# Kernel tuning notes

Measured on AMD Instinct MI355X. Metric: run time of the kernel, lower is better.

## Reference

```python
import jax, jax.numpy as jnp
import numpy as np

LR = 0.1  # inner-loop learning rate from `param - 0.1 * grad`

D = 4096          # memory width d; key/val are (1, d) per docstring
CTX = 512         # loss_context_size: number of keys per update step


def setup_inputs() -> dict:
    key = jax.random.key(0)
    k1, k2, k3 = jax.random.split(key, 3)
    W = jax.random.normal(k1, (D, D), dtype=jnp.float32) / np.sqrt(D)
    keys = jax.random.normal(k2, (CTX, D), dtype=jnp.float32)
    vals = jax.random.normal(k3, (CTX, D), dtype=jnp.float32)
    return {"W": W, "keys": keys, "vals": vals}


def reference(W, keys, vals):
    # OneStep.forward: preds_i = functional_forward(key_i, (W,)) = key_i @ W,
    # loss = MSE(preds, vals); new_W = W - 0.1 * dloss/dW.
    # The per-key loop is batched into a single (CTX, D) x (D, D) matmul.
    def loss_fn(Wp):
        preds = keys @ Wp  # (CTX, D)
        return jnp.mean((preds - vals) ** 2)

    g = jax.grad(loss_fn)(W)
    return W - LR * g
```

## Files before the change

kernel.cpp:

```cpp
#include <hip/hip_runtime.h>
#include <hip/hip_bf16.h>


typedef __bf16 bf16_t;
typedef __bf16 bf16x8 __attribute__((ext_vector_type(8)));
typedef float f32x4 __attribute__((ext_vector_type(4)));

#define D_DIM 4096
#define CTX_N 512
#define UPD_SCALE 9.5367431640625e-8f

__device__ __forceinline__ void gld16(const bf16_t* g, bf16_t* l) {
    __builtin_amdgcn_global_load_lds(
        (const __attribute__((address_space(1))) void*)g,
        (__attribute__((address_space(3))) void*)l, 16, 0, 0);
}

__global__ __launch_bounds__(256) void t_conv(
    const float* __restrict__ src, bf16_t* __restrict__ dstT,
    bf16_t* __restrict__ dstN, int M, int N)
{
    __shared__ float tile[64 * 65];
    const int tid = threadIdx.x;
    const int C0 = blockIdx.x * 64;
    const int R0 = blockIdx.y * 64;
    const int r  = tid >> 2, cs = (tid & 3) * 16;

    const float* s = src + (size_t)(R0 + r) * N + C0 + cs;
    float f[16];
#pragma unroll
    for (int u = 0; u < 4; ++u) {
        const float4 v = ((const float4*)s)[u];
        f[4 * u + 0] = v.x; f[4 * u + 1] = v.y; f[4 * u + 2] = v.z; f[4 * u + 3] = v.w;
    }
#pragma unroll
    for (int u = 0; u < 16; ++u) tile[r * 65 + cs + u] = f[u];

    if (dstN) {
        bf16x8 v0, v1;
#pragma unroll
        for (int u = 0; u < 8; ++u) { v0[u] = (bf16_t)f[u]; v1[u] = (bf16_t)f[8 + u]; }
        bf16_t* d = dstN + (size_t)(R0 + r) * N + C0 + cs;
        *(bf16x8*)d = v0; *(bf16x8*)(d + 8) = v1;
    }
    __syncthreads();

    const int rr = tid >> 2, k0 = (tid & 3) * 16;
    bf16x8 o0, o1;
#pragma unroll
    for (int u = 0; u < 8; ++u) {
        o0[u] = (bf16_t)tile[(k0 + u) * 65 + rr];
        o1[u] = (bf16_t)tile[(k0 + 8 + u) * 65 + rr];
    }
    bf16_t* d = dstT + (size_t)(C0 + rr) * M + R0 + k0;
    *(bf16x8*)d = o0; *(bf16x8*)(d + 8) = o1;
}

__global__ __launch_bounds__(256) void k1_residual(
    const bf16_t* __restrict__ Wt, const bf16_t* __restrict__ Kb,
    const bf16_t* __restrict__ Vt, bf16_t* __restrict__ Rt)
{
    __shared__ __align__(16) bf16_t As[64 * 32];
    __shared__ __align__(16) bf16_t Bs[64 * 32];

    const int tid = threadIdx.x;
    const int j0 = blockIdx.x * 64;
    const int c0 = blockIdx.y * 64;
    const int lane = tid & 63, wave = tid >> 6;
    const int wm = (wave >> 1) * 32, wn = (wave & 1) * 32;
    const int l15 = lane & 15, quad = lane >> 4;

    f32x4 acc[2][2] = {};

    const int srow = tid >> 2, sseg = (tid & 3) * 8;
    const bf16_t* ga = Wt + (size_t)(j0 + srow) * D_DIM + sseg;
    const bf16_t* gb = Kb + (size_t)(c0 + srow) * D_DIM + sseg;
    bf16_t* la = (bf16_t*)((char*)As + tid * 16);
    bf16_t* lb = (bf16_t*)((char*)Bs + tid * 16);

    for (int kk = 0; kk < D_DIM; kk += 32) {
        gld16(ga + kk, la);
        gld16(gb + kk, lb);
        __syncthreads();
        const bf16x8 a0 = *(const bf16x8*)(As + (wm + 0  + l15) * 32 + quad * 8);
        const bf16x8 a1 = *(const bf16x8*)(As + (wm + 16 + l15) * 32 + quad * 8);
        const bf16x8 b0 = *(const bf16x8*)(Bs + (wn + 0  + l15) * 32 + quad * 8);
        const bf16x8 b1 = *(const bf16x8*)(Bs + (wn + 16 + l15) * 32 + quad * 8);
        acc[0][0] = __builtin_amdgcn_mfma_f32_16x16x32_bf16(a0, b0, acc[0][0], 0, 0, 0);
        acc[0][1] = __builtin_amdgcn_mfma_f32_16x16x32_bf16(a0, b1, acc[0][1], 0, 0, 0);
        acc[1][0] = __builtin_amdgcn_mfma_f32_16x16x32_bf16(a1, b0, acc[1][0], 0, 0, 0);
        acc[1][1] = __builtin_amdgcn_mfma_f32_16x16x32_bf16(a1, b1, acc[1][1], 0, 0, 0);
        __syncthreads();
    }

#pragma unroll
    for (int im = 0; im < 2; ++im)
#pragma unroll
        for (int in = 0; in < 2; ++in)
#pragma unroll
            for (int r = 0; r < 4; ++r) {
                const int j = j0 + wm + im * 16 + quad * 4 + r;
                const int c = c0 + wn + in * 16 + l15;
                const size_t idx = (size_t)j * CTX_N + c;
                Rt[idx] = (bf16_t)(acc[im][in][r] - (float)Vt[idx]);
            }
}

__global__ __launch_bounds__(256) void k2_update(
    const bf16_t* __restrict__ Kt, const bf16_t* __restrict__ Rt,
    const float* __restrict__ W, float* __restrict__ out)
{
    __shared__ __align__(16) bf16_t As[64 * 32];
    __shared__ __align__(16) bf16_t Bs[64 * 32];

    const int tid = threadIdx.x;
    const int j0 = blockIdx.x * 64;
    const int i0 = blockIdx.y * 64;
    const int lane = tid & 63, wave = tid >> 6;
    const int wm = (wave >> 1) * 32, wn = (wave & 1) * 32;
    const int l15 = lane & 15, quad = lane >> 4;

    f32x4 acc[2][2] = {};

    const int srow = tid >> 2, sseg = (tid & 3) * 8;
    const bf16_t* ga = Kt + (size_t)(i0 + srow) * CTX_N + sseg;
    const bf16_t* gb = Rt + (size_t)(j0 + srow) * CTX_N + sseg;
    bf16_t* la = (bf16_t*)((char*)As + tid * 16);
    bf16_t* lb = (bf16_t*)((char*)Bs + tid * 16);

    for (int cc = 0; cc < CTX_N; cc += 32) {
        gld16(ga + cc, la);
        gld16(gb + cc, lb);
        __syncthreads();
        const bf16x8 a0 = *(const bf16x8*)(As + (wm + 0  + l15) * 32 + quad * 8);
        const bf16x8 a1 = *(const bf16x8*)(As + (wm + 16 + l15) * 32 + quad * 8);
        const bf16x8 b0 = *(const bf16x8*)(Bs + (wn + 0  + l15) * 32 + quad * 8);
        const bf16x8 b1 = *(const bf16x8*)(Bs + (wn + 16 + l15) * 32 + quad * 8);
        acc[0][0] = __builtin_amdgcn_mfma_f32_16x16x32_bf16(a0, b0, acc[0][0], 0, 0, 0);
        acc[0][1] = __builtin_amdgcn_mfma_f32_16x16x32_bf16(a0, b1, acc[0][1], 0, 0, 0);
        acc[1][0] = __builtin_amdgcn_mfma_f32_16x16x32_bf16(a1, b0, acc[1][0], 0, 0, 0);
        acc[1][1] = __builtin_amdgcn_mfma_f32_16x16x32_bf16(a1, b1, acc[1][1], 0, 0, 0);
        __syncthreads();
    }

#pragma unroll
    for (int im = 0; im < 2; ++im)
#pragma unroll
        for (int in = 0; in < 2; ++in)
#pragma unroll
            for (int r = 0; r < 4; ++r) {
                const int i = i0 + wm + im * 16 + quad * 4 + r;
                const int j = j0 + wn + in * 16 + l15;
                const size_t idx = (size_t)i * D_DIM + j;
                out[idx] = W[idx] - UPD_SCALE * acc[im][in][r];
            }
}

extern "C" void kernel_launch(void* const* d_in, const int* in_sizes, int n_in,
                              void* d_out, int out_size, void* d_ws, size_t ws_size,
                              hipStream_t stream) {
    const float* W = (const float*)d_in[0];
    const float* K = (const float*)d_in[1];
    const float* V = (const float*)d_in[2];
    float* out = (float*)d_out;

    char* ws = (char*)d_ws;
    bf16_t* Wt = (bf16_t*)(ws);
    bf16_t* Kt = (bf16_t*)(ws + (size_t)32 * 1024 * 1024);
    bf16_t* Kb = (bf16_t*)(ws + (size_t)36 * 1024 * 1024);
    bf16_t* Vt = (bf16_t*)(ws + (size_t)40 * 1024 * 1024);
    bf16_t* Rt = (bf16_t*)(ws + (size_t)44 * 1024 * 1024);

    t_conv<<<dim3(64, 64), 256, 0, stream>>>(W, Wt, nullptr, D_DIM, D_DIM);
    t_conv<<<dim3(64, 8),  256, 0, stream>>>(K, Kt, Kb,      CTX_N, D_DIM);
    t_conv<<<dim3(64, 8),  256, 0, stream>>>(V, Vt, nullptr, CTX_N, D_DIM);
    k1_residual<<<dim3(64, 8),  256, 0, stream>>>(Wt, Kb, Vt, Rt);
    k2_update  <<<dim3(64, 64), 256, 0, stream>>>(Kt, Rt, W, out);
}
```

Baseline: 231.3 us.

## Enlarge GEMM tiles, stage update epilogue via LDS, merge K/V conversion launches

The residual GEMM now uses 128x64 tiles with a 64-wide k step, and the update GEMM uses 128x128 tiles with 4x4 MFMA fragments per wave. This gives more data reuse per LDS load and fewer block launches. The update epilogue stages accumulators through shared memory so W reads and output writes are coalesced float4 accesses. The K and V transpose-convert launches are merged into one grid. In exchange, register and LDS use rise, which lowers occupancy, and the residual GEMM now has only 256 blocks.

```diff
diff --git a/kernel.cpp b/kernel.cpp
--- a/kernel.cpp
+++ b/kernel.cpp
@@ -16,7 +16,7 @@
         (__attribute__((address_space(3))) void*)l, 16, 0, 0);
 }
 
-__global__ __launch_bounds__(256) void t_conv(
+__device__ __forceinline__ void t_body(
     const float* __restrict__ src, bf16_t* __restrict__ dstT,
     bf16_t* __restrict__ dstN, int M, int N)
 {
@@ -45,64 +45,89 @@
     }
     __syncthreads();
 
-    const int rr = tid >> 2, k0 = (tid & 3) * 16;
     bf16x8 o0, o1;
 #pragma unroll
     for (int u = 0; u < 8; ++u) {
-        o0[u] = (bf16_t)tile[(k0 + u) * 65 + rr];
-        o1[u] = (bf16_t)tile[(k0 + 8 + u) * 65 + rr];
-    }
-    bf16_t* d = dstT + (size_t)(C0 + rr) * M + R0 + k0;
+        o0[u] = (bf16_t)tile[(cs + u) * 65 + r];
+        o1[u] = (bf16_t)tile[(cs + 8 + u) * 65 + r];
+    }
+    bf16_t* d = dstT + (size_t)(C0 + r) * M + R0 + cs;
     *(bf16x8*)d = o0; *(bf16x8*)(d + 8) = o1;
 }
+
+__global__ __launch_bounds__(256) void t_conv_w(
+    const float* __restrict__ W, bf16_t* __restrict__ Wt)
+{
+    t_body(W, Wt, nullptr, D_DIM, D_DIM);
+}
+
+__global__ __launch_bounds__(256) void t_conv_kv(
+    const float* __restrict__ K, const float* __restrict__ V,
+    bf16_t* __restrict__ Kt, bf16_t* __restrict__ Kb, bf16_t* __restrict__ Vt)
+{
+    if (blockIdx.z == 0) t_body(K, Kt, Kb, CTX_N, D_DIM);
+    else                 t_body(V, Vt, nullptr, CTX_N, D_DIM);
+}
+
 
 __global__ __launch_bounds__(256) void k1_residual(
     const bf16_t* __restrict__ Wt, const bf16_t* __restrict__ Kb,
     const bf16_t* __restrict__ Vt, bf16_t* __restrict__ Rt)
 {
-    __shared__ __align__(16) bf16_t As[64 * 32];
-    __shared__ __align__(16) bf16_t Bs[64 * 32];
+    __shared__ __align__(16) bf16_t As[128 * 64];
+    __shared__ __align__(16) bf16_t Bs[64 * 64];
 
     const int tid = threadIdx.x;
-    const int j0 = blockIdx.x * 64;
+    const int j0 = blockIdx.x * 128;
     const int c0 = blockIdx.y * 64;
     const int lane = tid & 63, wave = tid >> 6;
-    const int wm = (wave >> 1) * 32, wn = (wave & 1) * 32;
+    const int wi = (wave >> 1) * 64, wc = (wave & 1) * 32;
     const int l15 = lane & 15, quad = lane >> 4;
 
-    f32x4 acc[2][2] = {};
-
-    const int srow = tid >> 2, sseg = (tid & 3) * 8;
-    const bf16_t* ga = Wt + (size_t)(j0 + srow) * D_DIM + sseg;
-    const bf16_t* gb = Kb + (size_t)(c0 + srow) * D_DIM + sseg;
+    f32x4 acc[4][2] = {};
+
+    const bf16_t* ga = Wt + (size_t)(j0 + (tid >> 3)) * D_DIM + (tid & 7) * 8;
+    const bf16_t* gb = Kb + (size_t)(c0 + (tid >> 3)) * D_DIM + (tid & 7) * 8;
     bf16_t* la = (bf16_t*)((char*)As + tid * 16);
     bf16_t* lb = (bf16_t*)((char*)Bs + tid * 16);
 
-    for (int kk = 0; kk < D_DIM; kk += 32) {
-        gld16(ga + kk, la);
-        gld16(gb + kk, lb);
-        __syncthreads();
-        const bf16x8 a0 = *(const bf16x8*)(As + (wm + 0  + l15) * 32 + quad * 8);
-        const bf16x8 a1 = *(const bf16x8*)(As + (wm + 16 + l15) * 32 + quad * 8);
-        const bf16x8 b0 = *(const bf16x8*)(Bs + (wn + 0  + l15) * 32 + quad * 8);
-        const bf16x8 b1 = *(const bf16x8*)(Bs + (wn + 16 + l15) * 32 + quad * 8);
-        acc[0][0] = __builtin_amdgcn_mfma_f32_16x16x32_bf16(a0, b0, acc[0][0], 0, 0, 0);
-        acc[0][1] = __builtin_amdgcn_mfma_f32_16x16x32_bf16(a0, b1, acc[0][1], 0, 0, 0);
-        acc[1][0] = __builtin_amdgcn_mfma_f32_16x16x32_bf16(a1, b0, acc[1][0], 0, 0, 0);
-        acc[1][1] = __builtin_amdgcn_mfma_f32_16x16x32_bf16(a1, b1, acc[1][1], 0, 0, 0);
-        __syncthreads();
-    }
-
-#pragma unroll
-    for (int im = 0; im < 2; ++im)
-#pragma unroll
-        for (int in = 0; in < 2; ++in)
+    for (int kk = 0; kk < D_DIM; kk += 64) {
+#pragma unroll
+        for (int c = 0; c < 4; ++c)
+            gld16(ga + kk + (size_t)(c * 32) * D_DIM, la + c * 2048);
+#pragma unroll
+        for (int c = 0; c < 2; ++c)
+            gld16(gb + kk + (size_t)(c * 32) * D_DIM, lb + c * 2048);
+        __syncthreads();
+#pragma unroll
+        for (int kh = 0; kh < 2; ++kh) {
+            bf16x8 a[4], b[2];
+#pragma unroll
+            for (int mi = 0; mi < 4; ++mi)
+                a[mi] = *(const bf16x8*)(As + (wi + mi * 16 + l15) * 64 + kh * 32 + quad * 8);
+#pragma unroll
+            for (int ni = 0; ni < 2; ++ni)
+                b[ni] = *(const bf16x8*)(Bs + (wc + ni * 16 + l15) * 64 + kh * 32 + quad * 8);
+#pragma unroll
+            for (int mi = 0; mi < 4; ++mi)
+#pragma unroll
+                for (int ni = 0; ni < 2; ++ni)
+                    acc[mi][ni] = __builtin_amdgcn_mfma_f32_16x16x32_bf16(
+                        a[mi], b[ni], acc[mi][ni], 0, 0, 0);
+        }
+        __syncthreads();
+    }
+
+#pragma unroll
+    for (int mi = 0; mi < 4; ++mi)
+#pragma unroll
+        for (int ni = 0; ni < 2; ++ni)
 #pragma unroll
             for (int r = 0; r < 4; ++r) {
-                const int j = j0 + wm + im * 16 + quad * 4 + r;
-                const int c = c0 + wn + in * 16 + l15;
+                const int j = j0 + wi + mi * 16 + quad * 4 + r;
+                const int c = c0 + wc + ni * 16 + l15;
                 const size_t idx = (size_t)j * CTX_N + c;
-                Rt[idx] = (bf16_t)(acc[im][in][r] - (float)Vt[idx]);
+                Rt[idx] = (bf16_t)(acc[mi][ni][r] - (float)Vt[idx]);
             }
 }
 
@@ -110,50 +135,77 @@
     const bf16_t* __restrict__ Kt, const bf16_t* __restrict__ Rt,
     const float* __restrict__ W, float* __restrict__ out)
 {
-    __shared__ __align__(16) bf16_t As[64 * 32];
-    __shared__ __align__(16) bf16_t Bs[64 * 32];
+    __shared__ __align__(16) bf16_t As[128 * 32];
+    __shared__ __align__(16) bf16_t Bs[128 * 32];
+    __shared__ __align__(16) float  ep[64 * 132];
 
     const int tid = threadIdx.x;
-    const int j0 = blockIdx.x * 64;
-    const int i0 = blockIdx.y * 64;
+    const int j0 = blockIdx.x * 128, i0 = blockIdx.y * 128;
     const int lane = tid & 63, wave = tid >> 6;
-    const int wm = (wave >> 1) * 32, wn = (wave & 1) * 32;
+    const int wi = (wave >> 1) * 64, wj = (wave & 1) * 64;
     const int l15 = lane & 15, quad = lane >> 4;
 
-    f32x4 acc[2][2] = {};
-
-    const int srow = tid >> 2, sseg = (tid & 3) * 8;
-    const bf16_t* ga = Kt + (size_t)(i0 + srow) * CTX_N + sseg;
-    const bf16_t* gb = Rt + (size_t)(j0 + srow) * CTX_N + sseg;
+    f32x4 acc[4][4] = {};
+
+    const bf16_t* ga = Kt + (size_t)(i0 + (tid >> 2)) * CTX_N + (tid & 3) * 8;
+    const bf16_t* gb = Rt + (size_t)(j0 + (tid >> 2)) * CTX_N + (tid & 3) * 8;
     bf16_t* la = (bf16_t*)((char*)As + tid * 16);
     bf16_t* lb = (bf16_t*)((char*)Bs + tid * 16);
 
     for (int cc = 0; cc < CTX_N; cc += 32) {
         gld16(ga + cc, la);
+        gld16(ga + cc + (size_t)64 * CTX_N, la + 64 * 32);
         gld16(gb + cc, lb);
-        __syncthreads();
-        const bf16x8 a0 = *(const bf16x8*)(As + (wm + 0  + l15) * 32 + quad * 8);
-        const bf16x8 a1 = *(const bf16x8*)(As + (wm + 16 + l15) * 32 + quad * 8);
-        const bf16x8 b0 = *(const bf16x8*)(Bs + (wn + 0  + l15) * 32 + quad * 8);
-        const bf16x8 b1 = *(const bf16x8*)(Bs + (wn + 16 + l15) * 32 + quad * 8);
-        acc[0][0] = __builtin_amdgcn_mfma_f32_16x16x32_bf16(a0, b0, acc[0][0], 0, 0, 0);
-        acc[0][1] = __builtin_amdgcn_mfma_f32_16x16x32_bf16(a0, b1, acc[0][1], 0, 0, 0);
-        acc[1][0] = __builtin_amdgcn_mfma_f32_16x16x32_bf16(a1, b0, acc[1][0], 0, 0, 0);
-        acc[1][1] = __builtin_amdgcn_mfma_f32_16x16x32_bf16(a1, b1, acc[1][1], 0, 0, 0);
-        __syncthreads();
-    }
-
-#pragma unroll
-    for (int im = 0; im < 2; ++im)
-#pragma unroll
-        for (int in = 0; in < 2; ++in)
-#pragma unroll
-            for (int r = 0; r < 4; ++r) {
-                const int i = i0 + wm + im * 16 + quad * 4 + r;
-                const int j = j0 + wn + in * 16 + l15;
-                const size_t idx = (size_t)i * D_DIM + j;
-                out[idx] = W[idx] - UPD_SCALE * acc[im][in][r];
+        gld16(gb + cc + (size_t)64 * CTX_N, lb + 64 * 32);
+        __syncthreads();
+        bf16x8 a[4], b[4];
+#pragma unroll
+        for (int mi = 0; mi < 4; ++mi)
+            a[mi] = *(const bf16x8*)(As + (wi + mi * 16 + l15) * 32 + quad * 8);
+#pragma unroll
+        for (int ni = 0; ni < 4; ++ni)
+            b[ni] = *(const bf16x8*)(Bs + (wj + ni * 16 + l15) * 32 + quad * 8);
+#pragma unroll
+        for (int mi = 0; mi < 4; ++mi)
+#pragma unroll
+            for (int ni = 0; ni < 4; ++ni)
+                acc[mi][ni] = __builtin_amdgcn_mfma_f32_16x16x32_bf16(
+                    a[mi], b[ni], acc[mi][ni], 0, 0, 0);
+        __syncthreads();
+    }
+
+#pragma unroll
+    for (int p = 0; p < 2; ++p) {
+        if ((wave >> 1) == p) {
+#pragma unroll
+            for (int mi = 0; mi < 4; ++mi)
+#pragma unroll
+                for (int ni = 0; ni < 4; ++ni)
+#pragma unroll
+                    for (int r = 0; r < 4; ++r)
+                        ep[(mi * 16 + quad * 4 + r) * 132 + wj + ni * 16 + l15] =
+                            acc[mi][ni][r];
+        }
+        __syncthreads();
+        {
+            const int row = tid >> 2, cb = (tid & 3) * 32;
+            const float* wrow = W   + (size_t)(i0 + p * 64 + row) * D_DIM + j0 + cb;
+            float*      orow = out + (size_t)(i0 + p * 64 + row) * D_DIM + j0 + cb;
+            const float* erow = ep + row * 132 + cb;
+#pragma unroll
+            for (int u = 0; u < 8; ++u) {
+                const float4 wv = ((const float4*)wrow)[u];
+                const float4 ev = ((const float4*)erow)[u];
+                float4 ov;
+                ov.x = wv.x - UPD_SCALE * ev.x;
+                ov.y = wv.y - UPD_SCALE * ev.y;
+                ov.z = wv.z - UPD_SCALE * ev.z;
+                ov.w = wv.w - UPD_SCALE * ev.w;
+                ((float4*)orow)[u] = ov;
             }
+        }
+        __syncthreads();
+    }
 }
 
 extern "C" void kernel_launch(void* const* d_in, const int* in_sizes, int n_in,
@@ -171,9 +223,8 @@
     bf16_t* Vt = (bf16_t*)(ws + (size_t)40 * 1024 * 1024);
     bf16_t* Rt = (bf16_t*)(ws + (size_t)44 * 1024 * 1024);
 
-    t_conv<<<dim3(64, 64), 256, 0, stream>>>(W, Wt, nullptr, D_DIM, D_DIM);
-    t_conv<<<dim3(64, 8),  256, 0, stream>>>(K, Kt, Kb,      CTX_N, D_DIM);
-    t_conv<<<dim3(64, 8),  256, 0, stream>>>(V, Vt, nullptr, CTX_N, D_DIM);
-    k1_residual<<<dim3(64, 8),  256, 0, stream>>>(Wt, Kb, Vt, Rt);
-    k2_update  <<<dim3(64, 64), 256, 0, stream>>>(Kt, Rt, W, out);
-}
+    t_conv_w <<<dim3(64, 64),    256, 0, stream>>>(W, Wt);
+    t_conv_kv<<<dim3(64, 8, 2),  256, 0, stream>>>(K, V, Kt, Kb, Vt);
+    k1_residual<<<dim3(32, 8),   256, 0, stream>>>(Wt, Kb, Vt, Rt);
+    k2_update  <<<dim3(32, 32),  256, 0, stream>>>(Kt, Rt, W, out);
+}
```

Measured after the change: 242.3 us. 4.8% more time.
